# Kernel tuning notes

Hardware: AMD Instinct MI355X
Metric: run time of the kernel (lower is better)

## Reference

```python
import jax, jax.numpy as jnp
import numpy as np

EPS = 1e-5  # torch BatchNorm1d default
WIDTH = 16


def _bn(x, g, b):
    # training-mode BatchNorm1d: batch mean, biased variance
    m = jnp.mean(x, axis=0)
    v = jnp.var(x, axis=0)
    return (x - m) * jax.lax.rsqrt(v + EPS) * g + b


def _lin(x, w, b):
    return x @ w.T + b


def setup_inputs() -> dict:
    key = jax.random.key(0)
    ks = jax.random.split(key, 32)
    N, W, P, U = 2_000_000, WIDTH, 8, 64

    def lin_init(kw, kb, out_f, in_f):
        bound = 1.0 / np.sqrt(in_f)
        w = jax.random.uniform(kw, (out_f, in_f), jnp.float32, -bound, bound)
        b = jax.random.uniform(kb, (out_f,), jnp.float32, -bound, bound)
        return w, b

    inp = {
        "pos_values": jax.random.normal(ks[0], (N, 2), jnp.float32),
        "partname_indices": jax.random.randint(ks[1], (N,), 0, P, jnp.int64)
        if jax.config.jax_enable_x64
        else jax.random.randint(ks[1], (N,), 0, P, jnp.int32),
        # BatchNorm affine params (5 BN layers)
        "bn0_g": jnp.ones((2,), jnp.float32), "bn0_b": jnp.zeros((2,), jnp.float32),
        "bn1_g": jnp.ones((W,), jnp.float32), "bn1_b": jnp.zeros((W,), jnp.float32),
        "bn2_g": jnp.ones((W,), jnp.float32), "bn2_b": jnp.zeros((W,), jnp.float32),
        "bn3_g": jnp.ones((W,), jnp.float32), "bn3_b": jnp.zeros((W,), jnp.float32),
        "bn4_g": jnp.ones((W,), jnp.float32), "bn4_b": jnp.zeros((W,), jnp.float32),
    }
    inp["w1"], inp["b1"] = lin_init(ks[2], ks[3], W, 2)
    inp["w2"], inp["b2"] = lin_init(ks[4], ks[5], W, W)
    inp["w3"], inp["b3"] = lin_init(ks[6], ks[7], W, W)
    inp["w4"], inp["b4"] = lin_init(ks[8], ks[9], W, W)
    inp["w5"], inp["b5"] = lin_init(ks[10], ks[11], W, W)
    inp["emb_table"] = jax.random.normal(ks[12], (P, W), jnp.float32)
    inp["wc"], inp["bc"] = lin_init(ks[13], ks[14], U, 2 * W)
    return inp


def reference(pos_values, partname_indices,
              bn0_g, bn0_b, bn1_g, bn1_b, bn2_g, bn2_b, bn3_g, bn3_b, bn4_g, bn4_b,
              w1, b1, w2, b2, w3, b3, w4, b4, w5, b5,
              emb_table, wc, bc):
    # selfpos_encoder: BN(2) -> Linear(2,16) -> ReLU
    h = jax.nn.relu(_lin(_bn(pos_values, bn0_g, bn0_b), w1, b1))  # [N,16]
    # ResBlock 1
    y = jax.nn.relu(_lin(_bn(h, bn1_g, bn1_b), w2, b2))
    y = jax.nn.relu(_lin(_bn(y, bn2_g, bn2_b), w3, b3))
    h = h + y
    # ResBlock 2
    y = jax.nn.relu(_lin(_bn(h, bn3_g, bn3_b), w4, b4))
    y = jax.nn.relu(_lin(_bn(y, bn4_g, bn4_b), w5, b5))
    h = h + y
    # concat with partname embedding, classify
    emb = jnp.concatenate([h, emb_table[partname_indices]], axis=-1)  # [N,32]
    return _lin(emb, wc, bc)  # [N,64]
```

## Files before the change

### kernel.cpp

```cpp
#include <hip/hip_runtime.h>
#include <math.h>


#define WG 256
#define GRID_STATS 1024
#define GRID_FINAL 2048

#define PARTIALS_OFF 0
#define PARAMS_OFF   (GRID_STATS * 32)
#define PW1 0
#define PB1 32
#define PW2 48
#define PB2 304
#define PW3 320
#define PB3 576
#define PW4 592
#define PB4 848
#define PW5 864
#define PB5 1120
#define PT2 1136

__device__ __forceinline__ void lin_relu16(const float* __restrict__ W,
                                           const float* __restrict__ B,
                                           const float x[16], float y[16]) {
  #pragma unroll
  for (int o = 0; o < 16; ++o) {
    float acc = B[o];
    #pragma unroll
    for (int i = 0; i < 16; ++i) acc = fmaf(W[o * 16 + i], x[i], acc);
    y[o] = fmaxf(acc, 0.f);
  }
}

template <int DEPTH>
__device__ __forceinline__ void forward_row(const float* __restrict__ P,
                                            float x0, float x1, float v[16]) {
  if (DEPTH == 0) {
    v[0] = x0; v[1] = x1;
    #pragma unroll
    for (int i = 2; i < 16; ++i) v[i] = 0.f;
    return;
  }
  float h[16];
  #pragma unroll
  for (int o = 0; o < 16; ++o)
    h[o] = fmaxf(fmaf(P[PW1 + 2 * o], x0, fmaf(P[PW1 + 2 * o + 1], x1, P[PB1 + o])), 0.f);
  if (DEPTH == 1) {
    #pragma unroll
    for (int i = 0; i < 16; ++i) v[i] = h[i];
    return;
  }
  float y[16];
  lin_relu16(P + PW2, P + PB2, h, y);
  if (DEPTH == 2) {
    #pragma unroll
    for (int i = 0; i < 16; ++i) v[i] = y[i];
    return;
  }
  float z[16];
  lin_relu16(P + PW3, P + PB3, y, z);
  #pragma unroll
  for (int o = 0; o < 16; ++o) h[o] += z[o];
  if (DEPTH == 3) {
    #pragma unroll
    for (int i = 0; i < 16; ++i) v[i] = h[i];
    return;
  }
  lin_relu16(P + PW4, P + PB4, h, y);
  if (DEPTH == 4) {
    #pragma unroll
    for (int i = 0; i < 16; ++i) v[i] = y[i];
    return;
  }
  lin_relu16(P + PW5, P + PB5, y, z);
  #pragma unroll
  for (int o = 0; o < 16; ++o) h[o] += z[o];
  #pragma unroll
  for (int i = 0; i < 16; ++i) v[i] = h[i];
}

template <int DEPTH>
__global__ __launch_bounds__(WG) void k_stats(const float* __restrict__ pos, int N,
                                              const float* __restrict__ P,
                                              float* __restrict__ partials) {
  constexpr int NC = (DEPTH == 0) ? 2 : 16;
  float s[16], q[16];
  #pragma unroll
  for (int c = 0; c < 16; ++c) { s[c] = 0.f; q[c] = 0.f; }
  const float2* pos2 = (const float2*)pos;
  for (int r = blockIdx.x * WG + threadIdx.x; r < N; r += GRID_STATS * WG) {
    float2 p = pos2[r];
    float v[16];
    forward_row<DEPTH>(P, p.x, p.y, v);
    #pragma unroll
    for (int c = 0; c < NC; ++c) { s[c] += v[c]; q[c] = fmaf(v[c], v[c], q[c]); }
  }
  __shared__ float redS[4][16], redQ[4][16];
  int lane = threadIdx.x & 63, wave = threadIdx.x >> 6;
  #pragma unroll
  for (int c = 0; c < 16; ++c) {
    float vs = s[c], vq = q[c];
    #pragma unroll
    for (int m = 1; m < 64; m <<= 1) {
      vs += __shfl_xor(vs, m, 64);
      vq += __shfl_xor(vq, m, 64);
    }
    if (lane == 0) { redS[wave][c] = vs; redQ[wave][c] = vq; }
  }
  __syncthreads();
  if (threadIdx.x < 16) {
    int c = threadIdx.x;
    partials[blockIdx.x * 32 + c]      = redS[0][c] + redS[1][c] + redS[2][c] + redS[3][c];
    partials[blockIdx.x * 32 + 16 + c] = redQ[0][c] + redQ[1][c] + redQ[2][c] + redQ[3][c];
  }
}

__global__ __launch_bounds__(WG) void k_fold(const float* __restrict__ partials,
                                             const float* __restrict__ gam,
                                             const float* __restrict__ bet,
                                             const float* __restrict__ W,
                                             const float* __restrict__ bias,
                                             int C, int O, float invN,
                                             float* __restrict__ Wf,
                                             float* __restrict__ bf) {
  __shared__ float red[8][32];
  __shared__ float colsum[32];
  __shared__ float scale[16], shift[16];
  int t = threadIdx.x;
  int c = t & 31, grp = t >> 5;
  float acc = 0.f;
  for (int bI = grp; bI < GRID_STATS; bI += 8) acc += partials[bI * 32 + c];
  red[grp][c] = acc;
  __syncthreads();
  if (t < 32) {
    float x = 0.f;
    #pragma unroll
    for (int g2 = 0; g2 < 8; ++g2) x += red[g2][t];
    colsum[t] = x;
  }
  __syncthreads();
  if (t < C) {
    float mean = colsum[t] * invN;
    float var  = colsum[16 + t] * invN - mean * mean;
    float sc   = gam[t] / sqrtf(var + 1e-5f);
    scale[t] = sc;
    shift[t] = bet[t] - mean * sc;
  }
  __syncthreads();
  for (int o = t; o < O; o += WG) {
    float a2 = bias[o];
    for (int cc = 0; cc < C; ++cc) {
      float w = W[o * C + cc];
      Wf[o * C + cc] = w * scale[cc];
      a2 = fmaf(w, shift[cc], a2);
    }
    bf[o] = a2;
  }
}

__global__ void k_table(const float* __restrict__ emb, const float* __restrict__ wc,
                        const float* __restrict__ bc, float* __restrict__ t2) {
  int t = threadIdx.x;
  int p = t >> 6, o = t & 63;
  float acc = bc[o];
  #pragma unroll
  for (int i = 0; i < 16; ++i) acc = fmaf(emb[p * 16 + i], wc[o * 32 + 16 + i], acc);
  t2[p * 64 + o] = acc;
}

__global__ __launch_bounds__(WG) void k_final(const float* __restrict__ pos,
                                              const int* __restrict__ idx,
                                              const float* __restrict__ P,
                                              const float* __restrict__ wc,
                                              float* __restrict__ out, int N) {
  __shared__ float sh[256][20];
  __shared__ int   sidx[256];
  __shared__ float4 st2[128];

  const int t = threadIdx.x;
  const int chunk = t & 15;
  const int rgrp  = t >> 4;

  if (t < 128) st2[t] = ((const float4*)(P + PT2))[t];

  float4 w4[16];
  #pragma unroll
  for (int i = 0; i < 16; ++i) {
    w4[i].x = wc[(chunk * 4 + 0) * 32 + i];
    w4[i].y = wc[(chunk * 4 + 1) * 32 + i];
    w4[i].z = wc[(chunk * 4 + 2) * 32 + i];
    w4[i].w = wc[(chunk * 4 + 3) * 32 + i];
  }

  const float2* pos2 = (const float2*)pos;

  for (int base = blockIdx.x * WG; base < N; base += gridDim.x * WG) {
    int r = base + t;
    if (r < N) {
      float2 p = pos2[r];
      float h3[16];
      forward_row<5>(P, p.x, p.y, h3);
      float4* row4 = (float4*)&sh[t][0];
      #pragma unroll
      for (int ii = 0; ii < 4; ++ii)
        row4[ii] = make_float4(h3[ii * 4 + 0], h3[ii * 4 + 1],
                               h3[ii * 4 + 2], h3[ii * 4 + 3]);
      sidx[t] = idx[r];
    }
    __syncthreads();

    #pragma unroll
    for (int k = 0; k < 16; ++k) {
      int rb = (k << 4) + rgrp;
      int rg = base + rb;
      if (rg < N) {
        float4 acc = st2[sidx[rb] * 16 + chunk];
        const float4* hrow = (const float4*)&sh[rb][0];
        #pragma unroll
        for (int ii = 0; ii < 4; ++ii) {
          float4 hv = hrow[ii];
          acc.x = fmaf(w4[ii * 4 + 0].x, hv.x, acc.x);
          acc.y = fmaf(w4[ii * 4 + 0].y, hv.x, acc.y);
          acc.z = fmaf(w4[ii * 4 + 0].z, hv.x, acc.z);
          acc.w = fmaf(w4[ii * 4 + 0].w, hv.x, acc.w);
          acc.x = fmaf(w4[ii * 4 + 1].x, hv.y, acc.x);
          acc.y = fmaf(w4[ii * 4 + 1].y, hv.y, acc.y);
          acc.z = fmaf(w4[ii * 4 + 1].z, hv.y, acc.z);
          acc.w = fmaf(w4[ii * 4 + 1].w, hv.y, acc.w);
          acc.x = fmaf(w4[ii * 4 + 2].x, hv.z, acc.x);
          acc.y = fmaf(w4[ii * 4 + 2].y, hv.z, acc.y);
          acc.z = fmaf(w4[ii * 4 + 2].z, hv.z, acc.z);
          acc.w = fmaf(w4[ii * 4 + 2].w, hv.z, acc.w);
          acc.x = fmaf(w4[ii * 4 + 3].x, hv.w, acc.x);
          acc.y = fmaf(w4[ii * 4 + 3].y, hv.w, acc.y);
          acc.z = fmaf(w4[ii * 4 + 3].z, hv.w, acc.z);
          acc.w = fmaf(w4[ii * 4 + 3].w, hv.w, acc.w);
        }
        ((float4*)(out + (size_t)rg * 64))[chunk] = acc;
      }
    }
    __syncthreads();
  }
}

extern "C" void kernel_launch(void* const* d_in, const int* in_sizes, int n_in,
                              void* d_out, int out_size, void* d_ws, size_t ws_size,
                              hipStream_t stream) {
  const float* pos = (const float*)d_in[0];
  const int*   idx = (const int*)d_in[1];
  const float* bn_g[5] = {(const float*)d_in[2], (const float*)d_in[4], (const float*)d_in[6],
                          (const float*)d_in[8], (const float*)d_in[10]};
  const float* bn_b[5] = {(const float*)d_in[3], (const float*)d_in[5], (const float*)d_in[7],
                          (const float*)d_in[9], (const float*)d_in[11]};
  const float* w[5] = {(const float*)d_in[12], (const float*)d_in[14], (const float*)d_in[16],
                       (const float*)d_in[18], (const float*)d_in[20]};
  const float* b[5] = {(const float*)d_in[13], (const float*)d_in[15], (const float*)d_in[17],
                       (const float*)d_in[19], (const float*)d_in[21]};
  const float* emb = (const float*)d_in[22];
  const float* wc  = (const float*)d_in[23];
  const float* bc  = (const float*)d_in[24];
  float* out = (float*)d_out;

  int N = in_sizes[0] / 2;
  float invN = 1.0f / (float)N;

  float* ws = (float*)d_ws;
  float* partials = ws + PARTIALS_OFF;
  float* P = ws + PARAMS_OFF;

  k_stats<0><<<GRID_STATS, WG, 0, stream>>>(pos, N, P, partials);
  k_fold<<<1, WG, 0, stream>>>(partials, bn_g[0], bn_b[0], w[0], b[0], 2, 16, invN,
                               P + PW1, P + PB1);
  k_stats<1><<<GRID_STATS, WG, 0, stream>>>(pos, N, P, partials);
  k_fold<<<1, WG, 0, stream>>>(partials, bn_g[1], bn_b[1], w[1], b[1], 16, 16, invN,
                               P + PW2, P + PB2);
  k_stats<2><<<GRID_STATS, WG, 0, stream>>>(pos, N, P, partials);
  k_fold<<<1, WG, 0, stream>>>(partials, bn_g[2], bn_b[2], w[2], b[2], 16, 16, invN,
                               P + PW3, P + PB3);
  k_stats<3><<<GRID_STATS, WG, 0, stream>>>(pos, N, P, partials);
  k_fold<<<1, WG, 0, stream>>>(partials, bn_g[3], bn_b[3], w[3], b[3], 16, 16, invN,
                               P + PW4, P + PB4);
  k_stats<4><<<GRID_STATS, WG, 0, stream>>>(pos, N, P, partials);
  k_fold<<<1, WG, 0, stream>>>(partials, bn_g[4], bn_b[4], w[4], b[4], 16, 16, invN,
                               P + PW5, P + PB5);
  k_table<<<1, 512, 0, stream>>>(emb, wc, bc, P + PT2);
  k_final<<<GRID_FINAL, WG, 0, stream>>>(pos, idx, P, wc, out, N);
}
```

Baseline: 1.933 ms.

## Stage folded MLP weights in LDS and process multiple rows per thread

The recompute passes now copy the folded layer parameters into shared memory and have each thread handle 2–4 rows at once. Each weight value loaded as a float4 is then reused across several rows, and position loads become float4 vectors. Each final-kernel block builds its own partname table instead of relying on a separate launch, and handles 512 rows per iteration. The costs are higher register pressure from the per-thread row batches, more LDS per block, and the table being recomputed by every block.

```diff
diff --git a/kernel.cpp b/kernel.cpp
--- a/kernel.cpp
+++ b/kernel.cpp
@@ -5,6 +5,8 @@
 #define WG 256
 #define GRID_STATS 1024
 #define GRID_FINAL 2048
+#define NPARAMS 1136
+#define TROWS 512
 
 #define PARTIALS_OFF 0
 #define PARAMS_OFF   (GRID_STATS * 32)
@@ -18,92 +20,163 @@
 #define PB4 848
 #define PW5 864
 #define PB5 1120
-#define PT2 1136
-
-__device__ __forceinline__ void lin_relu16(const float* __restrict__ W,
-                                           const float* __restrict__ B,
-                                           const float x[16], float y[16]) {
+
+template <int RB>
+__device__ __forceinline__ void lin_relu16_b(const float* WL, int wOff, int bOff,
+                                             const float x[RB][16], float y[RB][16]) {
   #pragma unroll
   for (int o = 0; o < 16; ++o) {
-    float acc = B[o];
-    #pragma unroll
-    for (int i = 0; i < 16; ++i) acc = fmaf(W[o * 16 + i], x[i], acc);
-    y[o] = fmaxf(acc, 0.f);
-  }
-}
-
-template <int DEPTH>
-__device__ __forceinline__ void forward_row(const float* __restrict__ P,
-                                            float x0, float x1, float v[16]) {
+    const float4* wr = (const float4*)(WL + wOff + o * 16);
+    const float4 wa = wr[0], wb = wr[1], wcc = wr[2], wd = wr[3];
+    const float bo = WL[bOff + o];
+    #pragma unroll
+    for (int r = 0; r < RB; ++r) {
+      float a = fmaf(wa.x, x[r][0], bo);
+      float b = wa.y * x[r][1];
+      a = fmaf(wa.z, x[r][2], a);  b = fmaf(wa.w, x[r][3], b);
+      a = fmaf(wb.x, x[r][4], a);  b = fmaf(wb.y, x[r][5], b);
+      a = fmaf(wb.z, x[r][6], a);  b = fmaf(wb.w, x[r][7], b);
+      a = fmaf(wcc.x, x[r][8], a); b = fmaf(wcc.y, x[r][9], b);
+      a = fmaf(wcc.z, x[r][10], a); b = fmaf(wcc.w, x[r][11], b);
+      a = fmaf(wd.x, x[r][12], a); b = fmaf(wd.y, x[r][13], b);
+      a = fmaf(wd.z, x[r][14], a); b = fmaf(wd.w, x[r][15], b);
+      y[r][o] = fmaxf(a + b, 0.f);
+    }
+  }
+}
+
+template <int DEPTH, int RB>
+__device__ __forceinline__ void forward_rows(const float* WL,
+                                             const float px[RB], const float py[RB],
+                                             float v[RB][16]) {
   if (DEPTH == 0) {
-    v[0] = x0; v[1] = x1;
-    #pragma unroll
-    for (int i = 2; i < 16; ++i) v[i] = 0.f;
-    return;
-  }
-  float h[16];
-  #pragma unroll
-  for (int o = 0; o < 16; ++o)
-    h[o] = fmaxf(fmaf(P[PW1 + 2 * o], x0, fmaf(P[PW1 + 2 * o + 1], x1, P[PB1 + o])), 0.f);
+    #pragma unroll
+    for (int r = 0; r < RB; ++r) {
+      v[r][0] = px[r]; v[r][1] = py[r];
+      #pragma unroll
+      for (int i = 2; i < 16; ++i) v[r][i] = 0.f;
+    }
+    return;
+  }
+  float h[RB][16];
+  #pragma unroll
+  for (int o = 0; o < 16; ++o) {
+    const float2 w01 = ((const float2*)(WL + PW1))[o];
+    const float b0 = WL[PB1 + o];
+    #pragma unroll
+    for (int r = 0; r < RB; ++r)
+      h[r][o] = fmaxf(fmaf(w01.x, px[r], fmaf(w01.y, py[r], b0)), 0.f);
+  }
   if (DEPTH == 1) {
     #pragma unroll
-    for (int i = 0; i < 16; ++i) v[i] = h[i];
-    return;
-  }
-  float y[16];
-  lin_relu16(P + PW2, P + PB2, h, y);
+    for (int r = 0; r < RB; ++r)
+      #pragma unroll
+      for (int i = 0; i < 16; ++i) v[r][i] = h[r][i];
+    return;
+  }
+  float y[RB][16];
+  lin_relu16_b<RB>(WL, PW2, PB2, h, y);
   if (DEPTH == 2) {
     #pragma unroll
-    for (int i = 0; i < 16; ++i) v[i] = y[i];
-    return;
-  }
-  float z[16];
-  lin_relu16(P + PW3, P + PB3, y, z);
-  #pragma unroll
-  for (int o = 0; o < 16; ++o) h[o] += z[o];
+    for (int r = 0; r < RB; ++r)
+      #pragma unroll
+      for (int i = 0; i < 16; ++i) v[r][i] = y[r][i];
+    return;
+  }
+  float z[RB][16];
+  lin_relu16_b<RB>(WL, PW3, PB3, y, z);
+  #pragma unroll
+  for (int r = 0; r < RB; ++r)
+    #pragma unroll
+    for (int o = 0; o < 16; ++o) h[r][o] += z[r][o];
   if (DEPTH == 3) {
     #pragma unroll
-    for (int i = 0; i < 16; ++i) v[i] = h[i];
-    return;
-  }
-  lin_relu16(P + PW4, P + PB4, h, y);
+    for (int r = 0; r < RB; ++r)
+      #pragma unroll
+      for (int i = 0; i < 16; ++i) v[r][i] = h[r][i];
+    return;
+  }
+  lin_relu16_b<RB>(WL, PW4, PB4, h, y);
   if (DEPTH == 4) {
     #pragma unroll
-    for (int i = 0; i < 16; ++i) v[i] = y[i];
-    return;
-  }
-  lin_relu16(P + PW5, P + PB5, y, z);
-  #pragma unroll
-  for (int o = 0; o < 16; ++o) h[o] += z[o];
-  #pragma unroll
-  for (int i = 0; i < 16; ++i) v[i] = h[i];
-}
-
-template <int DEPTH>
+    for (int r = 0; r < RB; ++r)
+      #pragma unroll
+      for (int i = 0; i < 16; ++i) v[r][i] = y[r][i];
+    return;
+  }
+  lin_relu16_b<RB>(WL, PW5, PB5, y, z);
+  #pragma unroll
+  for (int r = 0; r < RB; ++r)
+    #pragma unroll
+    for (int i = 0; i < 16; ++i) v[r][i] = h[r][i] + z[r][i];
+}
+
+template <int DEPTH, int RB>
 __global__ __launch_bounds__(WG) void k_stats(const float* __restrict__ pos, int N,
                                               const float* __restrict__ P,
                                               float* __restrict__ partials) {
+  __shared__ alignas(16) float WL[NPARAMS];
+  if (DEPTH > 0) {
+    for (int i = threadIdx.x; i < NPARAMS; i += WG) WL[i] = P[i];
+    __syncthreads();
+  }
   constexpr int NC = (DEPTH == 0) ? 2 : 16;
   float s[16], q[16];
   #pragma unroll
   for (int c = 0; c < 16; ++c) { s[c] = 0.f; q[c] = 0.f; }
-  const float2* pos2 = (const float2*)pos;
-  for (int r = blockIdx.x * WG + threadIdx.x; r < N; r += GRID_STATS * WG) {
-    float2 p = pos2[r];
-    float v[16];
-    forward_row<DEPTH>(P, p.x, p.y, v);
-    #pragma unroll
-    for (int c = 0; c < NC; ++c) { s[c] += v[c]; q[c] = fmaf(v[c], v[c], q[c]); }
-  }
+
+  const int stride = GRID_STATS * WG * RB;
+  for (int r0 = (blockIdx.x * WG + threadIdx.x) * RB; r0 < N; r0 += stride) {
+    const bool full = (r0 + RB <= N);
+    float px[RB], py[RB];
+    if (full) {
+      #pragma unroll
+      for (int j = 0; j < RB / 2; ++j) {
+        float4 v4 = *(const float4*)(pos + 2 * (r0 + 2 * j));
+        px[2 * j] = v4.x;     py[2 * j] = v4.y;
+        px[2 * j + 1] = v4.z; py[2 * j + 1] = v4.w;
+      }
+    } else {
+      #pragma unroll
+      for (int j = 0; j < RB; ++j) {
+        int r = r0 + j;
+        px[j] = (r < N) ? pos[2 * r] : 0.f;
+        py[j] = (r < N) ? pos[2 * r + 1] : 0.f;
+      }
+    }
+    float v[RB][16];
+    forward_rows<DEPTH, RB>(WL, px, py, v);
+    if (full) {
+      #pragma unroll
+      for (int j = 0; j < RB; ++j)
+        #pragma unroll
+        for (int c = 0; c < NC; ++c) {
+          s[c] += v[j][c];
+          q[c] = fmaf(v[j][c], v[j][c], q[c]);
+        }
+    } else {
+      #pragma unroll
+      for (int j = 0; j < RB; ++j) {
+        if (r0 + j < N) {
+          #pragma unroll
+          for (int c = 0; c < NC; ++c) {
+            s[c] += v[j][c];
+            q[c] = fmaf(v[j][c], v[j][c], q[c]);
+          }
+        }
+      }
+    }
+  }
+
   __shared__ float redS[4][16], redQ[4][16];
   int lane = threadIdx.x & 63, wave = threadIdx.x >> 6;
   #pragma unroll
   for (int c = 0; c < 16; ++c) {
     float vs = s[c], vq = q[c];
     #pragma unroll
-    for (int m = 1; m < 64; m <<= 1) {
-      vs += __shfl_xor(vs, m, 64);
-      vq += __shfl_xor(vq, m, 64);
+    for (int mm = 1; mm < 64; mm <<= 1) {
+      vs += __shfl_xor(vs, mm, 64);
+      vq += __shfl_xor(vq, mm, 64);
     }
     if (lane == 0) { redS[wave][c] = vs; redQ[wave][c] = vq; }
   }
@@ -158,30 +231,31 @@
   }
 }
 
-__global__ void k_table(const float* __restrict__ emb, const float* __restrict__ wc,
-                        const float* __restrict__ bc, float* __restrict__ t2) {
-  int t = threadIdx.x;
-  int p = t >> 6, o = t & 63;
-  float acc = bc[o];
-  #pragma unroll
-  for (int i = 0; i < 16; ++i) acc = fmaf(emb[p * 16 + i], wc[o * 32 + 16 + i], acc);
-  t2[p * 64 + o] = acc;
-}
-
 __global__ __launch_bounds__(WG) void k_final(const float* __restrict__ pos,
                                               const int* __restrict__ idx,
                                               const float* __restrict__ P,
                                               const float* __restrict__ wc,
+                                              const float* __restrict__ emb,
+                                              const float* __restrict__ bc,
                                               float* __restrict__ out, int N) {
-  __shared__ float sh[256][20];
-  __shared__ int   sidx[256];
+  __shared__ alignas(16) float WL[NPARAMS];
+  __shared__ alignas(16) float sh[TROWS][20];
+  __shared__ int sidx[TROWS];
   __shared__ float4 st2[128];
 
   const int t = threadIdx.x;
   const int chunk = t & 15;
   const int rgrp  = t >> 4;
 
-  if (t < 128) st2[t] = ((const float4*)(P + PT2))[t];
+  for (int i = t; i < NPARAMS; i += WG) WL[i] = P[i];
+
+  for (int s2 = t; s2 < 512; s2 += WG) {
+    int p = s2 >> 6, o = s2 & 63;
+    float acc = bc[o];
+    #pragma unroll
+    for (int i = 0; i < 16; ++i) acc = fmaf(emb[p * 16 + i], wc[o * 32 + 16 + i], acc);
+    ((float*)st2)[p * 64 + o] = acc;
+  }
 
   float4 w4[16];
   #pragma unroll
@@ -191,26 +265,39 @@
     w4[i].z = wc[(chunk * 4 + 2) * 32 + i];
     w4[i].w = wc[(chunk * 4 + 3) * 32 + i];
   }
-
-  const float2* pos2 = (const float2*)pos;
-
-  for (int base = blockIdx.x * WG; base < N; base += gridDim.x * WG) {
-    int r = base + t;
-    if (r < N) {
-      float2 p = pos2[r];
-      float h3[16];
-      forward_row<5>(P, p.x, p.y, h3);
-      float4* row4 = (float4*)&sh[t][0];
-      #pragma unroll
-      for (int ii = 0; ii < 4; ++ii)
-        row4[ii] = make_float4(h3[ii * 4 + 0], h3[ii * 4 + 1],
-                               h3[ii * 4 + 2], h3[ii * 4 + 3]);
-      sidx[t] = idx[r];
+  __syncthreads();
+
+  for (int base = blockIdx.x * TROWS; base < N; base += gridDim.x * TROWS) {
+    {
+      int r0 = base + 2 * t;
+      float px[2], py[2];
+      if (r0 + 2 <= N) {
+        float4 v4 = *(const float4*)(pos + 2 * r0);
+        px[0] = v4.x; py[0] = v4.y; px[1] = v4.z; py[1] = v4.w;
+      } else {
+        #pragma unroll
+        for (int j = 0; j < 2; ++j) {
+          int r = r0 + j;
+          px[j] = (r < N) ? pos[2 * r] : 0.f;
+          py[j] = (r < N) ? pos[2 * r + 1] : 0.f;
+        }
+      }
+      float v[2][16];
+      forward_rows<5, 2>(WL, px, py, v);
+      #pragma unroll
+      for (int j = 0; j < 2; ++j) {
+        float4* row4 = (float4*)&sh[2 * t + j][0];
+        row4[0] = make_float4(v[j][0],  v[j][1],  v[j][2],  v[j][3]);
+        row4[1] = make_float4(v[j][4],  v[j][5],  v[j][6],  v[j][7]);
+        row4[2] = make_float4(v[j][8],  v[j][9],  v[j][10], v[j][11]);
+        row4[3] = make_float4(v[j][12], v[j][13], v[j][14], v[j][15]);
+        sidx[2 * t + j] = (r0 + j < N) ? idx[r0 + j] : 0;
+      }
     }
     __syncthreads();
 
-    #pragma unroll
-    for (int k = 0; k < 16; ++k) {
+    #pragma unroll 4
+    for (int k = 0; k < TROWS / 16; ++k) {
       int rb = (k << 4) + rgrp;
       int rg = base + rb;
       if (rg < N) {
@@ -268,21 +355,20 @@
   float* partials = ws + PARTIALS_OFF;
   float* P = ws + PARAMS_OFF;
 
-  k_stats<0><<<GRID_STATS, WG, 0, stream>>>(pos, N, P, partials);
+  k_stats<0, 4><<<GRID_STATS, WG, 0, stream>>>(pos, N, P, partials);
   k_fold<<<1, WG, 0, stream>>>(partials, bn_g[0], bn_b[0], w[0], b[0], 2, 16, invN,
                                P + PW1, P + PB1);
-  k_stats<1><<<GRID_STATS, WG, 0, stream>>>(pos, N, P, partials);
+  k_stats<1, 4><<<GRID_STATS, WG, 0, stream>>>(pos, N, P, partials);
   k_fold<<<1, WG, 0, stream>>>(partials, bn_g[1], bn_b[1], w[1], b[1], 16, 16, invN,
                                P + PW2, P + PB2);
-  k_stats<2><<<GRID_STATS, WG, 0, stream>>>(pos, N, P, partials);
+  k_stats<2, 4><<<GRID_STATS, WG, 0, stream>>>(pos, N, P, partials);
   k_fold<<<1, WG, 0, stream>>>(partials, bn_g[2], bn_b[2], w[2], b[2], 16, 16, invN,
                                P + PW3, P + PB3);
-  k_stats<3><<<GRID_STATS, WG, 0, stream>>>(pos, N, P, partials);
+  k_stats<3, 2><<<GRID_STATS, WG, 0, stream>>>(pos, N, P, partials);
   k_fold<<<1, WG, 0, stream>>>(partials, bn_g[3], bn_b[3], w[3], b[3], 16, 16, invN,
                                P + PW4, P + PB4);
-  k_stats<4><<<GRID_STATS, WG, 0, stream>>>(pos, N, P, partials);
+  k_stats<4, 2><<<GRID_STATS, WG, 0, stream>>>(pos, N, P, partials);
   k_fold<<<1, WG, 0, stream>>>(partials, bn_g[4], bn_b[4], w[4], b[4], 16, 16, invN,
                                P + PW5, P + PB5);
-  k_table<<<1, 512, 0, stream>>>(emb, wc, bc, P + PT2);
-  k_final<<<GRID_FINAL, WG, 0, stream>>>(pos, idx, P, wc, out, N);
-}
+  k_final<<<GRID_FINAL, WG, 0, stream>>>(pos, idx, P, wc, emb, bc, out, N);
+}
```

After: 2.803 ms. 45.0% more time.
